# Kernel optimization log

Hardware: AMD Instinct MI355X
Metric: run time of the kernel (lower is better)

Reference implementation:

```python
import jax, jax.numpy as jnp
import numpy as np

DIMS = [1024, 2048, 1024, 1024]


def setup_inputs() -> dict:
    key = jax.random.key(0)
    ks = jax.random.split(key, 13)
    d_in, h1, h2, d_out = DIMS
    s = lambda k, shape, fan_in: jax.random.normal(k, shape, dtype=jnp.float32) / np.sqrt(fan_in)
    return {
        "x": jax.random.normal(ks[0], (4, 2048, d_in), dtype=jnp.float32),
        "w1": s(ks[1], (h1, d_in), d_in), "b1": jnp.zeros((h1,), jnp.float32),
        "w2": s(ks[2], (h2, h1), h1), "b2": jnp.zeros((h2,), jnp.float32),
        "wq": s(ks[3], (h2, h2), h2), "bq": jnp.zeros((h2,), jnp.float32),
        "wk": s(ks[4], (h2, h2), h2), "bk": jnp.zeros((h2,), jnp.float32),
        "wv": s(ks[5], (h2, h2), h2), "bv": jnp.zeros((h2,), jnp.float32),
        "wo": s(ks[6], (d_out, h2), h2), "bo": jnp.zeros((d_out,), jnp.float32),
    }


def reference(x, w1, b1, w2, b2, wq, bq, wk, bk, wv, bv, wo, bo):
    # MLP: Linear + ReLU twice (torch Linear: x @ W^T + b)
    h = jax.nn.relu(jnp.einsum('bsd,hd->bsh', x, w1) + b1)
    h = jax.nn.relu(jnp.einsum('bsh,eh->bse', h, w2) + b2)
    # Self-attention (single head over full hidden_dim)
    q = jnp.einsum('bse,fe->bsf', h, wq) + bq
    k = jnp.einsum('bse,fe->bsf', h, wk) + bk
    v = jnp.einsum('bse,fe->bsf', h, wv) + bv
    hidden_dim = wq.shape[0]
    scores = jnp.einsum('bsf,btf->bst', q, k) / jnp.sqrt(jnp.float32(hidden_dim))
    attn = jax.nn.softmax(scores, axis=-1)
    ctx = jnp.einsum('bst,btf->bsf', attn, v) + v  # residual with V
    return jnp.einsum('bsf,of->bso', ctx, wo) + bo
```

## Files before the change

### kernel.cpp

```cpp
#include <hip/hip_runtime.h>
#include <hip/hip_bf16.h>

typedef __bf16 bf16;
typedef bf16 bf16x8 __attribute__((ext_vector_type(8)));
typedef float f32x4 __attribute__((ext_vector_type(4)));

#define EPI_BIAS_RELU  0
#define EPI_BIAS_BF16  1
#define EPI_PLAIN_BF16 2
#define EPI_RESID      3
#define EPI_BIAS_F32   4

__device__ __forceinline__ void lds_load16(const bf16* g, bf16* l) {
  __builtin_amdgcn_global_load_lds((__attribute__((address_space(1))) void*)g,
                                   (__attribute__((address_space(3))) void*)l,
                                   16, 0, 0);
}

template<int N> __device__ __forceinline__ void vmw() {
  if constexpr (N == 0) asm volatile("s_waitcnt vmcnt(0)" ::: "memory");
  else if constexpr (N == 4) asm volatile("s_waitcnt vmcnt(4)" ::: "memory");
}
__device__ __forceinline__ void barrier() { asm volatile("s_barrier" ::: "memory"); }

__device__ __forceinline__ void xcd_map(int& bx, int& by, int& z) {
  const int gx = gridDim.x, gy = gridDim.y;
  const int Y8 = (gy * gridDim.z) >> 3;
  const int L = (blockIdx.z * gy + blockIdx.y) * gx + blockIdx.x;
  const int xcd = L & 7, j = L >> 3;
  bx = j % gx;
  const int yy = xcd * Y8 + j / gx;
  by = yy % gy;
  z  = yy / gy;
}

template<int EPI>
__global__ __launch_bounds__(256, 2)
void gemm2s(const bf16* __restrict__ A, const bf16* __restrict__ B,
            void* __restrict__ Cv, const float* __restrict__ bias,
            const bf16* __restrict__ resid,
            int K, int lda, int ldb, int ldc, int ldr,
            long long sAz, long long sBz, long long sCz, long long sRz)
{
  constexpr int BK = 64;
  constexpr int M_REP = 4, NH = 2;

  __shared__ __align__(16) bf16 lA[2][128 * BK];
  __shared__ __align__(16) bf16 lB[2][128 * BK];

  int bx, by, z;
  xcd_map(bx, by, z);

  const bf16* Ab = A + (size_t)z * sAz;
  const bf16* Bb = B + (size_t)z * sBz;
  const int row0 = by * 128, col0 = bx * 128;
  const int tid = threadIdx.x, w = tid >> 6, l = tid & 63;
  const int wr = w >> 1, wc = w & 1;

  const int srow = l >> 3, scb = (l & 7) ^ srow;
  const bf16* gA = Ab + (size_t)(row0 + w * 8 + srow) * lda + scb * 8;
  const bf16* gB = Bb + (size_t)(col0 + w * 8 + srow) * ldb + scb * 8;

  auto issueA = [&](int buf, int k0) {
#pragma unroll
    for (int i = 0; i < 4; i++)
      lds_load16(gA + (size_t)(i * 32) * lda + k0,
                 &lA[buf][(i * 32 + w * 8) * BK]);
  };
  auto issueB = [&](int buf, int k0) {
#pragma unroll
    for (int i = 0; i < 4; i++)
      lds_load16(gB + (size_t)(i * 32) * ldb + k0,
                 &lB[buf][(i * 32 + w * 8) * BK]);
  };

  const int fr = l & 15, fq = l >> 4, sw = fr & 7;
  bf16x8 aA[M_REP][2], bB0[NH][2], bB1[NH][2];
  f32x4 acc[M_REP][4] = {};

  auto readAfull = [&](int buf) {
#pragma unroll
    for (int m = 0; m < M_REP; m++) {
      const bf16* base = &lA[buf][(wr * 64 + m * 16 + fr) * BK];
#pragma unroll
      for (int kk = 0; kk < 2; kk++)
        aA[m][kk] = *(const bf16x8*)(base + ((kk * 4 + fq) ^ sw) * 8);
    }
  };
  auto readB = [&](bf16x8 (&dst)[NH][2], int buf, int h) {
#pragma unroll
    for (int nn = 0; nn < NH; nn++) {
      const bf16* base = &lB[buf][(wc * 64 + h * 32 + nn * 16 + fr) * BK];
#pragma unroll
      for (int kk = 0; kk < 2; kk++)
        dst[nn][kk] = *(const bf16x8*)(base + ((kk * 4 + fq) ^ sw) * 8);
    }
  };
  auto quad16 = [&](const bf16x8 (&b)[NH][2], int nBase) {
    __builtin_amdgcn_s_setprio(1);
#pragma unroll
    for (int kk = 0; kk < 2; kk++)
#pragma unroll
      for (int m = 0; m < M_REP; m++)
#pragma unroll
        for (int nh = 0; nh < NH; nh++)
          acc[m][nBase + nh] = __builtin_amdgcn_mfma_f32_16x16x32_bf16(
              aA[m][kk], b[nh][kk], acc[m][nBase + nh], 0, 0, 0);
    __builtin_amdgcn_s_setprio(0);
  };

  const int NT = K / BK;
  issueA(0, 0); issueB(0, 0); issueA(1, BK);
  vmw<4>();
  barrier();

  for (int t = 0; t < NT; t++) {
    const int cur = t & 1, nxt = cur ^ 1;
    const bool s1 = (t + 1 < NT), s2 = (t + 2 < NT);
    readAfull(cur);
    readB(bB0, cur, 0);
    if (s1) issueB(nxt, (t + 1) * BK);
    barrier();
    quad16(bB0, 0);
    barrier();
    readB(bB1, cur, 1);
    if (s2) { issueA(cur, (t + 2) * BK); vmw<4>(); }
    else vmw<0>();
    barrier();
    quad16(bB1, NH);
    barrier();
  }

#pragma unroll
  for (int m = 0; m < M_REP; m++) {
#pragma unroll
    for (int n = 0; n < 4; n++) {
      const int col = col0 + wc * 64 + n * 16 + fr;
#pragma unroll
      for (int j = 0; j < 4; j++) {
        const int rrow = row0 + wr * 64 + m * 16 + fq * 4 + j;
        const float val = acc[m][n][j];
        if constexpr (EPI == EPI_PLAIN_BF16) {
          bf16* Cp = (bf16*)Cv + (size_t)z * sCz;
          Cp[(size_t)rrow * ldc + col] = (bf16)val;
        } else if constexpr (EPI == EPI_BIAS_F32) {
          float* Cp = (float*)Cv;
          Cp[(size_t)rrow * ldc + col] = val + bias[col];
        } else if constexpr (EPI == EPI_BIAS_BF16) {
          bf16* Cp = (bf16*)Cv;
          Cp[(size_t)rrow * ldc + col] = (bf16)(val + bias[col]);
        } else if constexpr (EPI == EPI_BIAS_RELU) {
          bf16* Cp = (bf16*)Cv;
          Cp[(size_t)rrow * ldc + col] = (bf16)fmaxf(val + bias[col], 0.f);
        } else {
          bf16* Cp = (bf16*)Cv + (size_t)z * sCz;
          const bf16* Rp = resid + (size_t)z * sRz;
          Cp[(size_t)rrow * ldc + col] = (bf16)(val + (float)Rp[(size_t)rrow * ldr + col]);
        }
      }
    }
  }
}

__global__ __launch_bounds__(256)
void cast_all(const float* __restrict__ x,  const float* __restrict__ w1,
              const float* __restrict__ w2, const float* __restrict__ wq,
              const float* __restrict__ wk, const float* __restrict__ wv,
              const float* __restrict__ wo,
              bf16* __restrict__ xb, bf16* __restrict__ w1b,
              bf16* __restrict__ w2b, bf16* __restrict__ wqkb,
              bf16* __restrict__ wvb, bf16* __restrict__ wob) {
  const int b = blockIdx.x;
  const float* src; bf16* dst; int base; float scale = 1.f;
  if (b < 4096)      { src = x;  dst = xb;   base = b; }
  else if (b < 5120) { src = w1; dst = w1b;  base = b - 4096; }
  else if (b < 6144) { src = w2; dst = w2b;  base = b - 5120; }
  else if (b < 6656) { src = wq; dst = wqkb;              base = b - 6144; scale = 0.03125f; }
  else if (b < 7168) { src = wk; dst = wqkb + (1 << 20);  base = b - 6656; }
  else if (b < 7680) { src = wv; dst = wvb;  base = b - 7168; }
  else               { src = wo; dst = wob;  base = b - 7680; }
  const int i = base * 256 + threadIdx.x;
  const float4* p = (const float4*)src;
  float4 a = p[2 * i], c = p[2 * i + 1];
  bf16x8 o8;
  o8[0] = (bf16)(a.x * scale); o8[1] = (bf16)(a.y * scale);
  o8[2] = (bf16)(a.z * scale); o8[3] = (bf16)(a.w * scale);
  o8[4] = (bf16)(c.x * scale); o8[5] = (bf16)(c.y * scale);
  o8[6] = (bf16)(c.z * scale); o8[7] = (bf16)(c.w * scale);
  ((bf16x8*)dst)[i] = o8;
}

__global__ __launch_bounds__(256)
void pack_bias_qk(const float* __restrict__ bq, const float* __restrict__ bk,
                  float* __restrict__ o) {
  int i = blockIdx.x * 256 + threadIdx.x;
  o[i] = (i < 1024) ? bq[i] * 0.03125f : bk[i - 1024];
}

__global__ __launch_bounds__(256)
void transpose_bf16(const bf16* __restrict__ in, bf16* __restrict__ out,
                    int R, int C, int ldi,
                    long long inZ, long long outZ) {
  __shared__ bf16 t[64][72];
  const bf16* ib = in + (size_t)blockIdx.z * inZ;
  bf16* ob = out + (size_t)blockIdx.z * outZ;
  const int r0 = blockIdx.y * 64, c0 = blockIdx.x * 64;
  const int tid = threadIdx.x;
#pragma unroll
  for (int p = 0; p < 2; p++) {
    int r = p * 32 + tid / 8, cc = (tid % 8) * 8;
    bf16x8 vv = *(const bf16x8*)(ib + (size_t)(r0 + r) * ldi + c0 + cc);
#pragma unroll
    for (int j = 0; j < 8; j++) t[r][cc + j] = vv[j];
  }
  __syncthreads();
#pragma unroll
  for (int p = 0; p < 2; p++) {
    int r = p * 32 + tid / 8, cc = (tid % 8) * 8;
    bf16x8 o;
#pragma unroll
    for (int j = 0; j < 8; j++) o[j] = t[cc + j][r];
    *(bf16x8*)(ob + (size_t)(c0 + r) * R + r0 + cc) = o;
  }
}

__global__ __launch_bounds__(256)
void softmax_rows(bf16* __restrict__ S) {
  const size_t row = blockIdx.x;
  const int t = threadIdx.x, wv_ = t >> 6, ln = t & 63;
  bf16x8 v8 = ((const bf16x8*)(S + row * 2048))[t];
  float v[8];
#pragma unroll
  for (int j = 0; j < 8; j++) v[j] = (float)v8[j];
  float m = v[0];
#pragma unroll
  for (int j = 1; j < 8; j++) m = fmaxf(m, v[j]);
  for (int o = 32; o; o >>= 1) m = fmaxf(m, __shfl_xor(m, o));
  __shared__ float redm[4], reds[4];
  if (ln == 0) redm[wv_] = m;
  __syncthreads();
  m = fmaxf(fmaxf(redm[0], redm[1]), fmaxf(redm[2], redm[3]));
  float e[8], s = 0.f;
#pragma unroll
  for (int j = 0; j < 8; j++) { e[j] = __expf(v[j] - m); s += e[j]; }
  for (int o = 32; o; o >>= 1) s += __shfl_xor(s, o);
  if (ln == 0) reds[wv_] = s;
  __syncthreads();
  s = reds[0] + reds[1] + reds[2] + reds[3];
  const float inv = 1.f / s;
  bf16x8 o8;
#pragma unroll
  for (int j = 0; j < 8; j++) o8[j] = (bf16)(e[j] * inv);
  ((bf16x8*)(S + row * 2048))[t] = o8;
}

extern "C" void kernel_launch(void* const* d_in, const int* in_sizes, int n_in,
                              void* d_out, int out_size, void* d_ws, size_t ws_size,
                              hipStream_t stream) {
  const float* x  = (const float*)d_in[0];
  const float* w1 = (const float*)d_in[1];
  const float* b1 = (const float*)d_in[2];
  const float* w2 = (const float*)d_in[3];
  const float* b2 = (const float*)d_in[4];
  const float* wq = (const float*)d_in[5];
  const float* bq = (const float*)d_in[6];
  const float* wk = (const float*)d_in[7];
  const float* bk = (const float*)d_in[8];
  const float* wv = (const float*)d_in[9];
  const float* bv = (const float*)d_in[10];
  const float* wo = (const float*)d_in[11];
  const float* bo = (const float*)d_in[12];
  float* out = (float*)d_out;

  char* ws = (char*)d_ws;
  const size_t MB = 1024ull * 1024ull;
  if (ws_size < 130 * MB) return;

  bf16* w1b  = (bf16*)(ws + 0 * MB);
  bf16* w2b  = (bf16*)(ws + 4 * MB);
  bf16* wqkb = (bf16*)(ws + 8 * MB);
  bf16* wvb  = (bf16*)(ws + 12 * MB);
  bf16* wob  = (bf16*)(ws + 14 * MB);
  float* bqk = (float*)(ws + 16 * MB);
  bf16* xb  = (bf16*)(ws + 17 * MB);
  bf16* h1  = (bf16*)(ws + 33 * MB);
  bf16* h   = (bf16*)(ws + 65 * MB);
  bf16* qk  = (bf16*)(ws + 81 * MB);
  bf16* vb  = (bf16*)(ws + 113 * MB);
  bf16* vT  = (bf16*)(ws + 17 * MB);
  bf16* S   = (bf16*)(ws + 33 * MB);
  bf16* ctx = (bf16*)(ws + 65 * MB);

  cast_all<<<8192, 256, 0, stream>>>(x, w1, w2, wq, wk, wv, wo,
                                     xb, w1b, w2b, wqkb, wvb, wob);
  pack_bias_qk<<<8, 256, 0, stream>>>(bq, bk, bqk);

  gemm2s<EPI_BIAS_RELU><<<dim3(16, 64, 1), 256, 0, stream>>>(
      xb, w1b, h1, b1, nullptr, 1024, 1024, 1024, 2048, 0, 0, 0, 0, 0);
  gemm2s<EPI_BIAS_RELU><<<dim3(8, 64, 1), 256, 0, stream>>>(
      h1, w2b, h, b2, nullptr, 2048, 2048, 2048, 1024, 0, 0, 0, 0, 0);
  gemm2s<EPI_BIAS_BF16><<<dim3(16, 64, 1), 256, 0, stream>>>(
      h, wqkb, qk, bqk, nullptr, 1024, 1024, 1024, 2048, 0, 0, 0, 0, 0);
  gemm2s<EPI_BIAS_BF16><<<dim3(8, 64, 1), 256, 0, stream>>>(
      h, wvb, vb, bv, nullptr, 1024, 1024, 1024, 1024, 0, 0, 0, 0, 0);
  transpose_bf16<<<dim3(16, 32, 4), 256, 0, stream>>>(
      vb, vT, 2048, 1024, 1024, 2048LL * 1024, 1024LL * 2048);
  gemm2s<EPI_PLAIN_BF16><<<dim3(16, 16, 4), 256, 0, stream>>>(
      qk, qk + 1024, S, nullptr, nullptr, 1024, 2048, 2048, 2048, 0,
      2048LL * 2048, 2048LL * 2048, 2048LL * 2048, 0);
  softmax_rows<<<8192, 256, 0, stream>>>(S);
  gemm2s<EPI_RESID><<<dim3(8, 16, 4), 256, 0, stream>>>(
      S, vT, ctx, nullptr, vb, 2048, 2048, 2048, 1024, 1024,
      2048LL * 2048, 1024LL * 2048, 2048LL * 1024, 2048LL * 1024);
  gemm2s<EPI_BIAS_F32><<<dim3(8, 64, 1), 256, 0, stream>>>(
      ctx, wob, out, bo, nullptr, 1024, 1024, 1024, 1024, 0, 0, 0, 0, 0);
}
```

Measured before the change: 266.1 us.

## Shrink GEMM K-tile to 32 with simpler pipeline and fuse QKV projection

```diff
diff --git a/kernel.cpp b/kernel.cpp
--- a/kernel.cpp
+++ b/kernel.cpp
@@ -20,6 +20,9 @@
 template<int N> __device__ __forceinline__ void vmw() {
   if constexpr (N == 0) asm volatile("s_waitcnt vmcnt(0)" ::: "memory");
   else if constexpr (N == 4) asm volatile("s_waitcnt vmcnt(4)" ::: "memory");
+}
+__device__ __forceinline__ void lgkm0() {
+  asm volatile("s_waitcnt lgkmcnt(0)" ::: "memory");
 }
 __device__ __forceinline__ void barrier() { asm volatile("s_barrier" ::: "memory"); }
 
@@ -35,15 +38,15 @@
 }
 
 template<int EPI>
-__global__ __launch_bounds__(256, 2)
-void gemm2s(const bf16* __restrict__ A, const bf16* __restrict__ B,
+__global__ __launch_bounds__(256, 4)
+void gemm3s(const bf16* __restrict__ A, const bf16* __restrict__ B,
             void* __restrict__ Cv, const float* __restrict__ bias,
             const bf16* __restrict__ resid,
             int K, int lda, int ldb, int ldc, int ldr,
             long long sAz, long long sBz, long long sCz, long long sRz)
 {
-  constexpr int BK = 64;
-  constexpr int M_REP = 4, NH = 2;
+  constexpr int BK = 32;
+  constexpr int M_REP = 4, N_REP = 4;
 
   __shared__ __align__(16) bf16 lA[2][128 * BK];
   __shared__ __align__(16) bf16 lB[2][128 * BK];
@@ -57,84 +60,73 @@
   const int tid = threadIdx.x, w = tid >> 6, l = tid & 63;
   const int wr = w >> 1, wc = w & 1;
 
-  const int srow = l >> 3, scb = (l & 7) ^ srow;
-  const bf16* gA = Ab + (size_t)(row0 + w * 8 + srow) * lda + scb * 8;
-  const bf16* gB = Bb + (size_t)(col0 + w * 8 + srow) * ldb + scb * 8;
-
-  auto issueA = [&](int buf, int k0) {
-#pragma unroll
-    for (int i = 0; i < 4; i++)
-      lds_load16(gA + (size_t)(i * 32) * lda + k0,
-                 &lA[buf][(i * 32 + w * 8) * BK]);
+  const int srow = l >> 2, scb = (l & 3) ^ ((l >> 3) & 3);
+  const bf16* gA = Ab + (size_t)(row0 + w * 16 + srow) * lda + scb * 8;
+  const bf16* gB = Bb + (size_t)(col0 + w * 16 + srow) * ldb + scb * 8;
+
+  auto issue = [&](int buf, int k0) {
+#pragma unroll
+    for (int i = 0; i < 2; i++)
+      lds_load16(gA + (size_t)(i * 64) * lda + k0,
+                 &lA[buf][(i * 64 + w * 16) * BK]);
+#pragma unroll
+    for (int i = 0; i < 2; i++)
+      lds_load16(gB + (size_t)(i * 64) * ldb + k0,
+                 &lB[buf][(i * 64 + w * 16) * BK]);
   };
-  auto issueB = [&](int buf, int k0) {
-#pragma unroll
-    for (int i = 0; i < 4; i++)
-      lds_load16(gB + (size_t)(i * 32) * ldb + k0,
-                 &lB[buf][(i * 32 + w * 8) * BK]);
-  };
-
-  const int fr = l & 15, fq = l >> 4, sw = fr & 7;
-  bf16x8 aA[M_REP][2], bB0[NH][2], bB1[NH][2];
-  f32x4 acc[M_REP][4] = {};
-
-  auto readAfull = [&](int buf) {
+
+  const int fr = l & 15, fq = l >> 4;
+  const int swb = (fr >> 1) & 3;
+
+  bf16x8 aA[M_REP], bB[N_REP];
+  f32x4 acc[M_REP][N_REP] = {};
+
+  auto readFrags = [&](int buf) {
 #pragma unroll
     for (int m = 0; m < M_REP; m++) {
-      const bf16* base = &lA[buf][(wr * 64 + m * 16 + fr) * BK];
-#pragma unroll
-      for (int kk = 0; kk < 2; kk++)
-        aA[m][kk] = *(const bf16x8*)(base + ((kk * 4 + fq) ^ sw) * 8);
+      const int r = wr * 64 + m * 16 + fr;
+      aA[m] = *(const bf16x8*)(&lA[buf][r * BK + ((fq ^ swb) * 8)]);
+    }
+#pragma unroll
+    for (int n = 0; n < N_REP; n++) {
+      const int r = wc * 64 + n * 16 + fr;
+      bB[n] = *(const bf16x8*)(&lB[buf][r * BK + ((fq ^ swb) * 8)]);
     }
   };
-  auto readB = [&](bf16x8 (&dst)[NH][2], int buf, int h) {
-#pragma unroll
-    for (int nn = 0; nn < NH; nn++) {
-      const bf16* base = &lB[buf][(wc * 64 + h * 32 + nn * 16 + fr) * BK];
-#pragma unroll
-      for (int kk = 0; kk < 2; kk++)
-        dst[nn][kk] = *(const bf16x8*)(base + ((kk * 4 + fq) ^ sw) * 8);
-    }
-  };
-  auto quad16 = [&](const bf16x8 (&b)[NH][2], int nBase) {
+  auto mfma16 = [&]() {
     __builtin_amdgcn_s_setprio(1);
 #pragma unroll
-    for (int kk = 0; kk < 2; kk++)
-#pragma unroll
-      for (int m = 0; m < M_REP; m++)
-#pragma unroll
-        for (int nh = 0; nh < NH; nh++)
-          acc[m][nBase + nh] = __builtin_amdgcn_mfma_f32_16x16x32_bf16(
-              aA[m][kk], b[nh][kk], acc[m][nBase + nh], 0, 0, 0);
+    for (int m = 0; m < M_REP; m++)
+#pragma unroll
+      for (int n = 0; n < N_REP; n++)
+        acc[m][n] = __builtin_amdgcn_mfma_f32_16x16x32_bf16(
+            aA[m], bB[n], acc[m][n], 0, 0, 0);
     __builtin_amdgcn_s_setprio(0);
   };
 
   const int NT = K / BK;
-  issueA(0, 0); issueB(0, 0); issueA(1, BK);
+  issue(0, 0);
+  issue(1, BK);
   vmw<4>();
   barrier();
 
   for (int t = 0; t < NT; t++) {
-    const int cur = t & 1, nxt = cur ^ 1;
-    const bool s1 = (t + 1 < NT), s2 = (t + 2 < NT);
-    readAfull(cur);
-    readB(bB0, cur, 0);
-    if (s1) issueB(nxt, (t + 1) * BK);
+    const int cur = t & 1;
+    const bool s2 = (t + 2 < NT);
+    readFrags(cur);
+    lgkm0();
     barrier();
-    quad16(bB0, 0);
-    barrier();
-    readB(bB1, cur, 1);
-    if (s2) { issueA(cur, (t + 2) * BK); vmw<4>(); }
-    else vmw<0>();
-    barrier();
-    quad16(bB1, NH);
+    if (s2) issue(cur, (t + 2) * BK);
+    mfma16();
+    if (s2) vmw<4>();
+    else if (t + 1 < NT) vmw<0>();
     barrier();
   }
 
 #pragma unroll
   for (int m = 0; m < M_REP; m++) {
 #pragma unroll
-    for (int n = 0; n < 4; n++) {
+    for (int n = 0; n < N_REP; n++) {
       const int col = col0 + wc * 64 + n * 16 + fr;
 #pragma unroll
       for (int j = 0; j < 4; j++) {
@@ -168,17 +160,17 @@
               const float* __restrict__ wk, const float* __restrict__ wv,
               const float* __restrict__ wo,
               bf16* __restrict__ xb, bf16* __restrict__ w1b,
-              bf16* __restrict__ w2b, bf16* __restrict__ wqkb,
-              bf16* __restrict__ wvb, bf16* __restrict__ wob) {
+              bf16* __restrict__ w2b, bf16* __restrict__ wqkvb,
+              bf16* __restrict__ wob) {
   const int b = blockIdx.x;
   const float* src; bf16* dst; int base; float scale = 1.f;
-  if (b < 4096)      { src = x;  dst = xb;   base = b; }
-  else if (b < 5120) { src = w1; dst = w1b;  base = b - 4096; }
-  else if (b < 6144) { src = w2; dst = w2b;  base = b - 5120; }
-  else if (b < 6656) { src = wq; dst = wqkb;              base = b - 6144; scale = 0.03125f; }
-  else if (b < 7168) { src = wk; dst = wqkb + (1 << 20);  base = b - 6656; }
-  else if (b < 7680) { src = wv; dst = wvb;  base = b - 7168; }
-  else               { src = wo; dst = wob;  base = b - 7680; }
+  if (b < 4096)      { src = x;  dst = xb;    base = b; }
+  else if (b < 5120) { src = w1; dst = w1b;   base = b - 4096; }
+  else if (b < 6144) { src = w2; dst = w2b;   base = b - 5120; }
+  else if (b < 6656) { src = wq; dst = wqkvb;               base = b - 6144; scale = 0.03125f; }
+  else if (b < 7168) { src = wk; dst = wqkvb + (1 << 20);   base = b - 6656; }
+  else if (b < 7680) { src = wv; dst = wqkvb + (2 << 20);   base = b - 7168; }
+  else               { src = wo; dst = wob;   base = b - 7680; }
   const int i = base * 256 + threadIdx.x;
   const float4* p = (const float4*)src;
   float4 a = p[2 * i], c = p[2 * i + 1];
@@ -191,10 +183,10 @@
 }
 
 __global__ __launch_bounds__(256)
-void pack_bias_qk(const float* __restrict__ bq, const float* __restrict__ bk,
-                  float* __restrict__ o) {
+void pack_bias_qkv(const float* __restrict__ bq, const float* __restrict__ bk,
+                   const float* __restrict__ bv, float* __restrict__ o) {
   int i = blockIdx.x * 256 + threadIdx.x;
-  o[i] = (i < 1024) ? bq[i] * 0.03125f : bk[i - 1024];
+  o[i] = (i < 1024) ? bq[i] * 0.03125f : (i < 2048 ? bk[i - 1024] : bv[i - 2048]);
 }
 
 __global__ __launch_bounds__(256)
@@ -276,42 +268,38 @@
   const size_t MB = 1024ull * 1024ull;
   if (ws_size < 130 * MB) return;
 
-  bf16* w1b  = (bf16*)(ws + 0 * MB);
-  bf16* w2b  = (bf16*)(ws + 4 * MB);
-  bf16* wqkb = (bf16*)(ws + 8 * MB);
-  bf16* wvb  = (bf16*)(ws + 12 * MB);
-  bf16* wob  = (bf16*)(ws + 14 * MB);
-  float* bqk = (float*)(ws + 16 * MB);
+  bf16* w1b   = (bf16*)(ws + 0 * MB);
+  bf16* w2b   = (bf16*)(ws + 4 * MB);
+  bf16* wqkvb = (bf16*)(ws + 8 * MB);
+  bf16* wob   = (bf16*)(ws + 14 * MB);
+  float* bqkv = (float*)(ws + 16 * MB);
   bf16* xb  = (bf16*)(ws + 17 * MB);
   bf16* h1  = (bf16*)(ws + 33 * MB);
   bf16* h   = (bf16*)(ws + 65 * MB);
-  bf16* qk  = (bf16*)(ws + 81 * MB);
-  bf16* vb  = (bf16*)(ws + 113 * MB);
+  bf16* qkv = (bf16*)(ws + 81 * MB);
   bf16* vT  = (bf16*)(ws + 17 * MB);
   bf16* S   = (bf16*)(ws + 33 * MB);
   bf16* ctx = (bf16*)(ws + 65 * MB);
 
   cast_all<<<8192, 256, 0, stream>>>(x, w1, w2, wq, wk, wv, wo,
-                                     xb, w1b, w2b, wqkb, wvb, wob);
-  pack_bias_qk<<<8, 256, 0, stream>>>(bq, bk, bqk);
-
-  gemm2s<EPI_BIAS_RELU><<<dim3(16, 64, 1), 256, 0, stream>>>(
+                                     xb, w1b, w2b, wqkvb, wob);
+  pack_bias_qkv<<<12, 256, 0, stream>>>(bq, bk, bv, bqkv);
+
+  gemm3s<EPI_BIAS_RELU><<<dim3(16, 64, 1), 256, 0, stream>>>(
       xb, w1b, h1, b1, nullptr, 1024, 1024, 1024, 2048, 0, 0, 0, 0, 0);
-  gemm2s<EPI_BIAS_RELU><<<dim3(8, 64, 1), 256, 0, stream>>>(
+  gemm3s<EPI_BIAS_RELU><<<dim3(8, 64, 1), 256, 0, stream>>>(
       h1, w2b, h, b2, nullptr, 2048, 2048, 2048, 1024, 0, 0, 0, 0, 0);
-  gemm2s<EPI_BIAS_BF16><<<dim3(16, 64, 1), 256, 0, stream>>>(
-      h, wqkb, qk, bqk, nullptr, 1024, 1024, 1024, 2048, 0, 0, 0, 0, 0);
-  gemm2s<EPI_BIAS_BF16><<<dim3(8, 64, 1), 256, 0, stream>>>(
-      h, wvb, vb, bv, nullptr, 1024, 1024, 1024, 1024, 0, 0, 0, 0, 0);
+  gemm3s<EPI_BIAS_BF16><<<dim3(24, 64, 1), 256, 0, stream>>>(
+      h, wqkvb, qkv, bqkv, nullptr, 1024, 1024, 1024, 3072, 0, 0, 0, 0, 0);
   transpose_bf16<<<dim3(16, 32, 4), 256, 0, stream>>>(
-      vb, vT, 2048, 1024, 1024, 2048LL * 1024, 1024LL * 2048);
-  gemm2s<EPI_PLAIN_BF16><<<dim3(16, 16, 4), 256, 0, stream>>>(
-      qk, qk + 1024, S, nullptr, nullptr, 1024, 2048, 2048, 2048, 0,
-      2048LL * 2048, 2048LL * 2048, 2048LL * 2048, 0);
+      qkv + 2048, vT, 2048, 1024, 3072, 2048LL * 3072, 1024LL * 2048);
+  gemm3s<EPI_PLAIN_BF16><<<dim3(16, 16, 4), 256, 0, stream>>>(
+      qkv, qkv + 1024, S, nullptr, nullptr, 1024, 3072, 3072, 2048, 0,
+      2048LL * 3072, 2048LL * 3072, 2048LL * 2048, 0);
   softmax_rows<<<8192, 256, 0, stream>>>(S);
-  gemm2s<EPI_RESID><<<dim3(8, 16, 4), 256, 0, stream>>>(
-      S, vT, ctx, nullptr, vb, 2048, 2048, 2048, 1024, 1024,
-      2048LL * 2048, 1024LL * 2048, 2048LL * 1024, 2048LL * 1024);
-  gemm2s<EPI_BIAS_F32><<<dim3(8, 64, 1), 256, 0, stream>>>(
+  gemm3s<EPI_RESID><<<dim3(8, 16, 4), 256, 0, stream>>>(
+      S, vT, ctx, nullptr, qkv + 2048, 2048, 2048, 2048, 1024, 3072,
+      2048LL * 2048, 1024LL * 2048, 2048LL * 1024, 2048LL * 3072);
+  gemm3s<EPI_BIAS_F32><<<dim3(8, 64, 1), 256, 0, stream>>>(
       ctx, wob, out, bo, nullptr, 1024, 1024, 1024, 1024, 0, 0, 0, 0, 0);
 }
```

After: 296.4 us. +11.4%, slower.

## Fold Wq·Wk and Wv·Wo weight products to shrink attention GEMMs

Applied to the files above, without the earlier changes.

```diff
diff --git a/kernel.cpp b/kernel.cpp
--- a/kernel.cpp
+++ b/kernel.cpp
@@ -5,11 +5,11 @@
 typedef bf16 bf16x8 __attribute__((ext_vector_type(8)));
 typedef float f32x4 __attribute__((ext_vector_type(4)));
 
-#define EPI_BIAS_RELU  0
-#define EPI_BIAS_BF16  1
-#define EPI_PLAIN_BF16 2
-#define EPI_RESID      3
-#define EPI_BIAS_F32   4
+#define EPI_BIAS_RELU      0
+#define EPI_BIAS_BF16      1
+#define EPI_PLAIN_BF16     2
+#define EPI_RESID_BIAS_F32 3
+#define EPI_BIAS_F32       4
 
 __device__ __forceinline__ void lds_load16(const bf16* g, bf16* l) {
   __builtin_amdgcn_global_load_lds((__attribute__((address_space(1))) void*)g,
@@ -39,7 +39,7 @@
 void gemm2s(const bf16* __restrict__ A, const bf16* __restrict__ B,
             void* __restrict__ Cv, const float* __restrict__ bias,
             const bf16* __restrict__ resid,
-            int K, int lda, int ldb, int ldc, int ldr,
+            int K, int lda, int ldb, int ldc, int ldr, int biasZ,
             long long sAz, long long sBz, long long sCz, long long sRz)
 {
   constexpr int BK = 64;
@@ -131,6 +131,7 @@
     barrier();
   }
 
+  const float* bz = bias ? bias + (size_t)z * biasZ : nullptr;
 #pragma unroll
   for (int m = 0; m < M_REP; m++) {
 #pragma unroll
@@ -145,17 +146,18 @@
           Cp[(size_t)rrow * ldc + col] = (bf16)val;
         } else if constexpr (EPI == EPI_BIAS_F32) {
           float* Cp = (float*)Cv;
-          Cp[(size_t)rrow * ldc + col] = val + bias[col];
+          Cp[(size_t)rrow * ldc + col] = val + bz[col];
         } else if constexpr (EPI == EPI_BIAS_BF16) {
-          bf16* Cp = (bf16*)Cv;
-          Cp[(size_t)rrow * ldc + col] = (bf16)(val + bias[col]);
+          bf16* Cp = (bf16*)Cv + (size_t)z * sCz;
+          Cp[(size_t)rrow * ldc + col] = (bf16)(val + bz[col]);
         } else if constexpr (EPI == EPI_BIAS_RELU) {
           bf16* Cp = (bf16*)Cv;
-          Cp[(size_t)rrow * ldc + col] = (bf16)fmaxf(val + bias[col], 0.f);
+          Cp[(size_t)rrow * ldc + col] = (bf16)fmaxf(val + bz[col], 0.f);
         } else {
-          bf16* Cp = (bf16*)Cv + (size_t)z * sCz;
+          float* Cp = (float*)Cv + (size_t)z * sCz;
           const bf16* Rp = resid + (size_t)z * sRz;
-          Cp[(size_t)rrow * ldc + col] = (bf16)(val + (float)Rp[(size_t)rrow * ldr + col]);
+          Cp[(size_t)rrow * ldc + col] =
+              val + (float)Rp[(size_t)rrow * ldr + col] + bz[col];
         }
       }
     }
@@ -168,16 +170,16 @@
               const float* __restrict__ wk, const float* __restrict__ wv,
               const float* __restrict__ wo,
               bf16* __restrict__ xb, bf16* __restrict__ w1b,
-              bf16* __restrict__ w2b, bf16* __restrict__ wqkb,
-              bf16* __restrict__ wvb, bf16* __restrict__ wob) {
+              bf16* __restrict__ w2b, bf16* __restrict__ w3,
+              bf16* __restrict__ wob) {
   const int b = blockIdx.x;
   const float* src; bf16* dst; int base; float scale = 1.f;
   if (b < 4096)      { src = x;  dst = xb;   base = b; }
   else if (b < 5120) { src = w1; dst = w1b;  base = b - 4096; }
   else if (b < 6144) { src = w2; dst = w2b;  base = b - 5120; }
-  else if (b < 6656) { src = wq; dst = wqkb;              base = b - 6144; scale = 0.03125f; }
-  else if (b < 7168) { src = wk; dst = wqkb + (1 << 20);  base = b - 6656; }
-  else if (b < 7680) { src = wv; dst = wvb;  base = b - 7168; }
+  else if (b < 6656) { src = wq; dst = w3;               base = b - 6144; scale = 0.03125f; }
+  else if (b < 7168) { src = wv; dst = w3 + (1 << 20);   base = b - 6656; }
+  else if (b < 7680) { src = wk; dst = w3 + (2 << 20);   base = b - 7168; }
   else               { src = wo; dst = wob;  base = b - 7680; }
   const int i = base * 256 + threadIdx.x;
   const float4* p = (const float4*)src;
@@ -191,10 +193,23 @@
 }
 
 __global__ __launch_bounds__(256)
-void pack_bias_qk(const float* __restrict__ bq, const float* __restrict__ bk,
-                  float* __restrict__ o) {
-  int i = blockIdx.x * 256 + threadIdx.x;
-  o[i] = (i < 1024) ? bq[i] * 0.03125f : bk[i - 1024];
+void matvec_bias(const float* __restrict__ bq, const float* __restrict__ wk,
+                 const float* __restrict__ wo, const float* __restrict__ bv,
+                 float* __restrict__ bcbvo) {
+  const int b = blockIdx.x, t = threadIdx.x;
+  if (b < 4) {
+    const int e = b * 256 + t;
+    float acc = 0.f;
+    for (int f = 0; f < 1024; f++)
+      acc += bq[f] * 0.03125f * wk[(size_t)f * 1024 + e];
+    bcbvo[e] = acc;
+  } else {
+    const int o = (b - 4) * 256 + t;
+    float acc = 0.f;
+    for (int f = 0; f < 1024; f++)
+      acc += wo[(size_t)o * 1024 + f] * bv[f];
+    bcbvo[1024 + o] = acc;
+  }
 }
 
 __global__ __launch_bounds__(256)
@@ -271,47 +286,48 @@
   const float* wo = (const float*)d_in[11];
   const float* bo = (const float*)d_in[12];
   float* out = (float*)d_out;
+  (void)bk;
 
   char* ws = (char*)d_ws;
   const size_t MB = 1024ull * 1024ull;
   if (ws_size < 130 * MB) return;
 
-  bf16* w1b  = (bf16*)(ws + 0 * MB);
-  bf16* w2b  = (bf16*)(ws + 4 * MB);
-  bf16* wqkb = (bf16*)(ws + 8 * MB);
-  bf16* wvb  = (bf16*)(ws + 12 * MB);
-  bf16* wob  = (bf16*)(ws + 14 * MB);
-  float* bqk = (float*)(ws + 16 * MB);
-  bf16* xb  = (bf16*)(ws + 17 * MB);
-  bf16* h1  = (bf16*)(ws + 33 * MB);
-  bf16* h   = (bf16*)(ws + 65 * MB);
-  bf16* qk  = (bf16*)(ws + 81 * MB);
-  bf16* vb  = (bf16*)(ws + 113 * MB);
-  bf16* vT  = (bf16*)(ws + 17 * MB);
-  bf16* S   = (bf16*)(ws + 33 * MB);
-  bf16* ctx = (bf16*)(ws + 65 * MB);
+  bf16* w1b = (bf16*)(ws + 0 * MB);
+  bf16* w2b = (bf16*)(ws + 4 * MB);
+  bf16* w3  = (bf16*)(ws + 8 * MB);
+  bf16* T4  = (bf16*)(ws + 14 * MB);
+  bf16* WW  = (bf16*)(ws + 22 * MB);
+  float* bcbvo = (float*)(ws + 26 * MB);
+  bf16* xb  = (bf16*)(ws + 27 * MB);
+  bf16* h1  = (bf16*)(ws + 43 * MB);
+  bf16* h   = (bf16*)(ws + 75 * MB);
+  bf16* hq  = (bf16*)(ws + 91 * MB);
+  bf16* g   = (bf16*)(ws + 107 * MB);
+  bf16* S   = (bf16*)(ws + 43 * MB);
+  bf16* gT  = (bf16*)(ws + 27 * MB);
 
   cast_all<<<8192, 256, 0, stream>>>(x, w1, w2, wq, wk, wv, wo,
-                                     xb, w1b, w2b, wqkb, wvb, wob);
-  pack_bias_qk<<<8, 256, 0, stream>>>(bq, bk, bqk);
-
+                                     xb, w1b, w2b, w3, T4 + (3 << 20));
+  transpose_bf16<<<dim3(16, 16, 3), 256, 0, stream>>>(
+      w3, T4, 1024, 1024, 1024, 1 << 20, 1 << 20);
+  matvec_bias<<<8, 256, 0, stream>>>(bq, wk, wo, bv, bcbvo);
+  gemm2s<EPI_PLAIN_BF16><<<dim3(8, 8, 2), 256, 0, stream>>>(
+      T4 + (2 << 20), T4, WW, nullptr, nullptr,
+      1024, 1024, 1024, 1024, 0, 0, 1 << 20, 1 << 20, 1 << 20, 0);
   gemm2s<EPI_BIAS_RELU><<<dim3(16, 64, 1), 256, 0, stream>>>(
-      xb, w1b, h1, b1, nullptr, 1024, 1024, 1024, 2048, 0, 0, 0, 0, 0);
+      xb, w1b, h1, b1, nullptr, 1024, 1024, 1024, 2048, 0, 0, 0, 0, 0, 0);
   gemm2s<EPI_BIAS_RELU><<<dim3(8, 64, 1), 256, 0, stream>>>(
-      h1, w2b, h, b2, nullptr, 2048, 2048, 2048, 1024, 0, 0, 0, 0, 0);
-  gemm2s<EPI_BIAS_BF16><<<dim3(16, 64, 1), 256, 0, stream>>>(
-      h, wqkb, qk, bqk, nullptr, 1024, 1024, 1024, 2048, 0, 0, 0, 0, 0);
-  gemm2s<EPI_BIAS_BF16><<<dim3(8, 64, 1), 256, 0, stream>>>(
-      h, wvb, vb, bv, nullptr, 1024, 1024, 1024, 1024, 0, 0, 0, 0, 0);
+      h1, w2b, h, b2, nullptr, 2048, 2048, 2048, 1024, 0, 0, 0, 0, 0, 0);
+  gemm2s<EPI_BIAS_BF16><<<dim3(8, 64, 2), 256, 0, stream>>>(
+      h, WW, hq, bcbvo, nullptr, 1024, 1024, 1024, 1024, 0, 1024,
+      0, 1 << 20, 8LL << 20, 0);
+  gemm2s<EPI_PLAIN_BF16><<<dim3(16, 16, 4), 256, 0, stream>>>(
+      hq, h, S, nullptr, nullptr, 1024, 1024, 1024, 2048, 0, 0,
+      2048LL * 1024, 2048LL * 1024, 2048LL * 2048, 0);
+  softmax_rows<<<8192, 256, 0, stream>>>(S);
   transpose_bf16<<<dim3(16, 32, 4), 256, 0, stream>>>(
-      vb, vT, 2048, 1024, 1024, 2048LL * 1024, 1024LL * 2048);
-  gemm2s<EPI_PLAIN_BF16><<<dim3(16, 16, 4), 256, 0, stream>>>(
-      qk, qk + 1024, S, nullptr, nullptr, 1024, 2048, 2048, 2048, 0,
-      2048LL * 2048, 2048LL * 2048, 2048LL * 2048, 0);
-  softmax_rows<<<8192, 256, 0, stream>>>(S);
-  gemm2s<EPI_RESID><<<dim3(8, 16, 4), 256, 0, stream>>>(
-      S, vT, ctx, nullptr, vb, 2048, 2048, 2048, 1024, 1024,
-      2048LL * 2048, 1024LL * 2048, 2048LL * 1024, 2048LL * 1024);
-  gemm2s<EPI_BIAS_F32><<<dim3(8, 64, 1), 256, 0, stream>>>(
-      ctx, wob, out, bo, nullptr, 1024, 1024, 1024, 1024, 0, 0, 0, 0, 0);
-}
+      g, gT, 2048, 1024, 1024, 2048LL * 1024, 1024LL * 2048);
+  gemm2s<EPI_RESID_BIAS_F32><<<dim3(8, 16, 4), 256, 0, stream>>>(
+      S, gT, out, bo, g, 2048, 2048, 2048, 1024, 1024, 0,
+      2048LL * 2048, 2048LL * 1024, 2048LL * 1024, 2048LL * 1024);
+}
```

After: 271.0 us. No clear change (+1.9%).
